# Kernel optimization log

Measured on AMD Instinct MI355X. Metric: run time of the kernel, lower is better.

The kernel has to match this reference:

```python
import jax, jax.numpy as jnp
import numpy as np

D_MODEL = 1024
FEED = 4096
HEADS = 16
EPS = 1e-5


def _ln(x, g, b):
    mu = jnp.mean(x, axis=-1, keepdims=True)
    var = jnp.var(x, axis=-1, keepdims=True)
    return (x - mu) * jax.lax.rsqrt(var + EPS) * g + b


def setup_inputs() -> dict:
    key = jax.random.key(0)
    ks = jax.random.split(key, 8)
    s = 0.02
    return {
        "src": jax.random.normal(ks[0], (8, 512, D_MODEL), jnp.float32),
        "wq": jax.random.normal(ks[1], (D_MODEL, D_MODEL), jnp.float32) * s,
        "bq": jnp.zeros((D_MODEL,), jnp.float32),
        "wk": jax.random.normal(ks[2], (D_MODEL, D_MODEL), jnp.float32) * s,
        "bk": jnp.zeros((D_MODEL,), jnp.float32),
        "wv": jax.random.normal(ks[3], (D_MODEL, D_MODEL), jnp.float32) * s,
        "bv": jnp.zeros((D_MODEL,), jnp.float32),
        "g1": jnp.ones((D_MODEL,), jnp.float32),
        "be1": jnp.zeros((D_MODEL,), jnp.float32),
        "w1": jax.random.normal(ks[4], (D_MODEL, FEED), jnp.float32) * s,
        "b1": jnp.zeros((FEED,), jnp.float32),
        "w2": jax.random.normal(ks[5], (FEED, D_MODEL), jnp.float32) * s,
        "b2": jnp.zeros((D_MODEL,), jnp.float32),
        "g2": jnp.ones((D_MODEL,), jnp.float32),
        "be2": jnp.zeros((D_MODEL,), jnp.float32),
    }


def reference(src, wq, bq, wk, bk, wv, bv, g1, be1, w1, b1, w2, b2, g2, be2):
    bs, seq, d = src.shape
    dk = d // HEADS
    q = src @ wq + bq
    k = src @ wk + bk
    v = src @ wv + bv
    # [B, H, S, dk]
    q = q.reshape(bs, seq, HEADS, dk).transpose(0, 2, 1, 3)
    k = k.reshape(bs, seq, HEADS, dk).transpose(0, 2, 1, 3)
    v = v.reshape(bs, seq, HEADS, dk).transpose(0, 2, 1, 3)
    scores = jnp.einsum('bhqd,bhkd->bhqk', q, k)  # no mask (src_mask unused in original)
    att = jax.nn.softmax(scores / jnp.sqrt(jnp.float32(dk)), axis=-1)
    ctx = jnp.einsum('bhqk,bhkd->bhqd', att, v)
    ctx = ctx.transpose(0, 2, 1, 3).reshape(bs, seq, d)  # concat heads
    x = _ln(ctx + src, g1, be1)
    # FFN (dropout = identity at eval)
    h = jax.nn.relu(x @ w1 + b1)
    y = h @ w2 + b2
    return _ln(y + x, g2, be2)
```

## Files before the change

kernel.cpp:

```cpp
#include <hip/hip_runtime.h>
#include <hip/hip_bf16.h>
#include <stdint.h>

#define DM   1024
#define FF   4096
#define NH   16
#define DK   64
#define SEQ  512
#define NTOK 4096

typedef __attribute__((ext_vector_type(8))) unsigned short ushort8;
typedef __attribute__((ext_vector_type(4))) unsigned short ushort4v;
typedef __attribute__((ext_vector_type(8))) short bf16x8;
typedef __attribute__((ext_vector_type(4))) float f32x4;

__device__ __forceinline__ float bf2f(unsigned short u) {
  union { unsigned int i; float f; } v; v.i = ((unsigned int)u) << 16; return v.f;
}
__device__ __forceinline__ unsigned short f2bf(float f) {
  union { float fl; unsigned int i; } v; v.fl = f;
  v.i += 0x7fffu + ((v.i >> 16) & 1u);
  return (unsigned short)(v.i >> 16);
}

__device__ __forceinline__ void gload16(const unsigned short* g, unsigned short* l) {
  __builtin_amdgcn_global_load_lds(
      (const __attribute__((address_space(1))) unsigned int*)g,
      (__attribute__((address_space(3))) unsigned int*)l, 16, 0, 0);
}

__global__ __launch_bounds__(256)
void prep_kernel(const float* __restrict__ src, unsigned short* __restrict__ srcb,
                 const float* __restrict__ wq, const float* __restrict__ wk,
                 const float* __restrict__ wv, unsigned short* __restrict__ WqkvT,
                 const float* __restrict__ w1, unsigned short* __restrict__ W1T,
                 const float* __restrict__ w2, unsigned short* __restrict__ W2T,
                 const float* __restrict__ bq, const float* __restrict__ bk,
                 const float* __restrict__ bv, float* __restrict__ bqkv) {
  const int z = blockIdx.x;
  const int tid = threadIdx.x;
  if (z < 4096) {
    const long i = ((long)z * 256 + tid) * 4;
    f32x4 v = *(const f32x4*)(src + i);
    ushort4v o;
#pragma unroll
    for (int j = 0; j < 4; j++) o[j] = f2bf(v[j]);
    *(ushort4v*)(srcb + i) = o;
    return;
  }
  if (z >= 15360) {
    const int i = (z - 15360) * 256 + tid;
    if (i < 3072)
      bqkv[i] = (i < 1024) ? bq[i] : ((i < 2048) ? bk[i - 1024] : bv[i - 2048]);
    return;
  }
  const float* in;
  unsigned short* out;
  int ldin, ldout;
  long r0, c0;
  if (z < 7168) {
    const int w = (z - 4096) >> 10;
    const int t = (z - 4096) & 1023;
    in = (w == 0) ? wq : (w == 1) ? wk : wv;
    out = WqkvT + (long)w * 1024 * 1024;
    ldin = 1024; ldout = 1024;
    r0 = (long)(t >> 5) * 32; c0 = (long)(t & 31) * 32;
  } else if (z < 11264) {
    const int t = z - 7168;
    in = w1; out = W1T; ldin = 4096; ldout = 1024;
    r0 = (long)(t >> 7) * 32; c0 = (long)(t & 127) * 32;
  } else {
    const int t = z - 11264;
    in = w2; out = W2T; ldin = 1024; ldout = 4096;
    r0 = (long)(t >> 5) * 32; c0 = (long)(t & 31) * 32;
  }
  __shared__ unsigned short tile[32][33];
  const int tx = tid & 31, ty = tid >> 5;
#pragma unroll
  for (int i = 0; i < 4; i++)
    tile[ty + i * 8][tx] = f2bf(in[(r0 + ty + i * 8) * ldin + c0 + tx]);
  __syncthreads();
#pragma unroll
  for (int i = 0; i < 4; i++)
    out[(c0 + ty + i * 8) * ldout + r0 + tx] = tile[tx][ty + i * 8];
}

template <bool RELU, bool PARTIAL, bool VOUT>
__global__ __launch_bounds__(512, 2)
void gemm256(const unsigned short* __restrict__ A, int lda,
             const unsigned short* __restrict__ B, int ldb,
             const float* __restrict__ bias,
             unsigned short* __restrict__ C,
             unsigned short* __restrict__ P1,
             unsigned short* __restrict__ P2,
             unsigned short* __restrict__ P3,
             int ldc, int nTN) {
  __shared__ unsigned short sm[65536];
  const int tid = threadIdx.x;
  const int lane = tid & 63;
  const int wid = tid >> 6;
  const int wr = wid >> 2, wc = wid & 3;
  const int kgrp = wid >> 2;

  const unsigned int T = gridDim.x;
  const unsigned int q8 = T >> 3;
  const unsigned int x = blockIdx.x;
  const unsigned int swz = (x & 7) * q8 + (x >> 3);
  const long bm = (long)(swz / nTN) * 256;
  const long bn = (long)(swz % nTN) * 256;
  const long kbase = (long)blockIdx.y * 1024;

  f32x4 acc[8][4];
#pragma unroll
  for (int mf = 0; mf < 8; mf++)
#pragma unroll
    for (int nf = 0; nf < 4; nf++) acc[mf][nf] = f32x4{0.f, 0.f, 0.f, 0.f};

  const int strow = tid >> 2;
  const int scol = (((tid & 3) ^ ((tid >> 3) & 3)) << 3);
  const unsigned short* pA = A + (bm + strow) * lda + kbase + scol;
  const unsigned short* pB = B + (bn + strow) * ldb + kbase + scol;
  unsigned short* dA = sm + tid * 8;
  unsigned short* dB = sm + 32768 + tid * 8;

  const int g = lane >> 4;
  int offA[8], offB[4];
#pragma unroll
  for (int mf = 0; mf < 8; mf++) {
    const int rm = wr * 128 + mf * 16 + (lane & 15);
    offA[mf] = rm * 32 + ((g ^ ((rm >> 1) & 3)) << 3);
  }
#pragma unroll
  for (int nf = 0; nf < 4; nf++) {
    const int rb = wc * 64 + nf * 16 + (lane & 15);
    offB[nf] = rb * 32 + ((g ^ ((rb >> 1) & 3)) << 3);
  }

#define GA(kt, ks, rh, bu) gload16(pA + (long)(rh) * 128 * lda + (kt) * 64 + (ks) * 32, \
                                   dA + (bu) * 16384 + (ks) * 8192 + (rh) * 4096)
#define GB(kt, ks, rh, bu) gload16(pB + (long)(rh) * 128 * ldb + (kt) * 64 + (ks) * 32, \
                                   dB + (bu) * 16384 + (ks) * 8192 + (rh) * 4096)
#define MF16(AR, BR, MO)                                                      \
  do {                                                                        \
    __builtin_amdgcn_s_setprio(1);                                            \
    _Pragma("unroll")                                                         \
    for (int mf = 0; mf < 4; mf++)                                            \
      _Pragma("unroll")                                                       \
      for (int nf = 0; nf < 4; nf++)                                          \
        acc[(MO) + mf][nf] = __builtin_amdgcn_mfma_f32_16x16x32_bf16(         \
            AR[mf], BR[nf], acc[(MO) + mf][nf], 0, 0, 0);                     \
    __builtin_amdgcn_s_setprio(0);                                            \
  } while (0)

  GA(0, 0, 0, 0); GA(0, 0, 1, 0); GA(0, 1, 0, 0); GA(0, 1, 1, 0);
  GB(0, 0, 0, 0); GB(0, 0, 1, 0); GB(0, 1, 0, 0); GB(0, 1, 1, 0);

  for (int t = 0; t < 16; ++t) {
    const int c = t & 1, n2 = c ^ 1;
    const int k1 = t + 1;
    const unsigned short* smAc = sm + c * 16384;
    const unsigned short* smBc = sm + 32768 + c * 16384;
    bf16x8 a_[4], bcur[4];
    const int ks0off = kgrp * 8192;
    const int ks1off = (1 - kgrp) * 8192;

    GA(k1, 0, 0, n2); GA(k1, 0, 1, n2);
    asm volatile("s_waitcnt vmcnt(2)\ns_barrier" ::: "memory");
#pragma unroll
    for (int nf = 0; nf < 4; nf++) bcur[nf] = *(const bf16x8*)(smBc + ks0off + offB[nf]);
#pragma unroll
    for (int mf = 0; mf < 4; mf++) a_[mf] = *(const bf16x8*)(smAc + ks0off + offA[mf]);
    MF16(a_, bcur, 0);
    GA(k1, 1, 0, n2); GA(k1, 1, 1, n2);
#pragma unroll
    for (int mf = 0; mf < 4; mf++) a_[mf] = *(const bf16x8*)(smAc + ks0off + offA[4 + mf]);
    asm volatile("s_barrier" ::: "memory");
    MF16(a_, bcur, 4);
    GB(k1, 0, 0, n2); GB(k1, 0, 1, n2);
#pragma unroll
    for (int nf = 0; nf < 4; nf++) bcur[nf] = *(const bf16x8*)(smBc + ks1off + offB[nf]);
#pragma unroll
    for (int mf = 0; mf < 4; mf++) a_[mf] = *(const bf16x8*)(smAc + ks1off + offA[mf]);
    asm volatile("s_barrier" ::: "memory");
    MF16(a_, bcur, 0);
    GB(k1, 1, 0, n2); GB(k1, 1, 1, n2);
#pragma unroll
    for (int mf = 0; mf < 4; mf++) a_[mf] = *(const bf16x8*)(smAc + ks1off + offA[4 + mf]);
    asm volatile("s_waitcnt lgkmcnt(0)\ns_barrier" ::: "memory");
    MF16(a_, bcur, 4);
  }
#undef GA
#undef GB
#undef MF16

  asm volatile("s_waitcnt vmcnt(0)" ::: "memory");

  if (VOUT && bn >= 2048) {
    const int b  = (int)(bm >> 9);
    const int s0 = (int)(bm & 511);
    const int lcol = wc * 64 + (lane & 15);
    const int lrow = wr * 128 + ((lane >> 4) << 2);
#pragma unroll
    for (int nf = 0; nf < 4; nf++) {
      const int gcol = (int)bn + lcol + nf * 16;
      const float bv = bias[gcol];
      const int gc = gcol - 2048;
      const int h = gc >> 6, d = gc & 63;
      unsigned short* vbase = P1 + ((long)(b * 16 + h) * 64 + d) * 512;
#pragma unroll
      for (int mf = 0; mf < 8; mf++) {
        const int s = s0 + lrow + mf * 16;
        ushort4v o;
#pragma unroll
        for (int i = 0; i < 4; i++) o[i] = f2bf(acc[mf][nf][i] + bv);
        *(ushort4v*)(vbase + s) = o;
      }
    }
    return;
  }

  unsigned short* Cw = C;
  if (PARTIAL) {
    const int kc = blockIdx.y;
    Cw = (kc == 0) ? C : (kc == 1) ? P1 : (kc == 2) ? P2 : P3;
  }

  __syncthreads();
  {
    const int lrow = wr * 128 + ((lane >> 4) << 2);
    const int lcol = wc * 64 + (lane & 15);
#pragma unroll
    for (int nf = 0; nf < 4; nf++) {
      const int col = lcol + nf * 16;
      const float bv = PARTIAL ? 0.f : bias[bn + col];
#pragma unroll
      for (int mf = 0; mf < 8; mf++) {
#pragma unroll
        for (int i = 0; i < 4; i++) {
          float v = acc[mf][nf][i] + bv;
          if (RELU) v = fmaxf(v, 0.f);
          sm[(lrow + mf * 16 + i) * 256 + col] = f2bf(v);
        }
      }
    }
  }
  __syncthreads();
  const int srow = tid >> 5;
  const int scol8 = (tid & 31) * 8;
#pragma unroll
  for (int p = 0; p < 16; ++p) {
    const int r = p * 16 + srow;
    ushort8 vrow = *(const ushort8*)(sm + r * 256 + scol8);
    *(ushort8*)(&Cw[(bm + r) * ldc + bn + scol8]) = vrow;
  }
}

__global__ __launch_bounds__(256)
void attn_kernel(const unsigned short* __restrict__ QKV,
                 const unsigned short* __restrict__ Vt,
                 unsigned short* __restrict__ CTX) {
  const int lin = blockIdx.x;
  const int xcd = lin & 7;
  const int slot = lin >> 3;
  const int bh = xcd + 8 * (slot >> 3);
  const int qt = slot & 7;
  const int b = bh >> 4, h = bh & 15;
  const int tid = threadIdx.x;
  const int lane = tid & 63;
  const int wid = tid >> 6;

  __shared__ unsigned short Ks[64][72];
  __shared__ unsigned short Vs[64][72];
  __shared__ unsigned short Ps[4][16][72];

  const int qrow0 = qt * 64 + wid * 16;
  const unsigned short* Qb = QKV + (long)(b * SEQ + qrow0) * 3072 + h * 64;
  bf16x8 aq[2];
#pragma unroll
  for (int ks = 0; ks < 2; ks++)
    aq[ks] = *(const bf16x8*)(Qb + (long)(lane & 15) * 3072 + ks * 32 +
                              (lane >> 4) * 8);

  f32x4 acc_o[4];
#pragma unroll
  for (int n = 0; n < 4; n++) acc_o[n] = f32x4{0.f, 0.f, 0.f, 0.f};
  float rsum[4] = {0.f, 0.f, 0.f, 0.f};

  const int sr = tid >> 3;
  const int sc = (tid & 7) * 8;
  const unsigned short* Kg = QKV + (long)(b * SEQ) * 3072 + 1024 + h * 64 + sc;
  const unsigned short* Vg = Vt + (long)bh * (DK * SEQ) + sc;

  ushort8 kr0 = *(const ushort8*)(Kg + (long)sr * 3072);
  ushort8 kr1 = *(const ushort8*)(Kg + (long)(sr + 32) * 3072);
  ushort8 vr0 = *(const ushort8*)(Vg + (long)sr * SEQ);
  ushort8 vr1 = *(const ushort8*)(Vg + (long)(sr + 32) * SEQ);

#pragma unroll
  for (int c = 0; c < 8; ++c) {
    __syncthreads();
    *(ushort8*)(&Ks[sr][sc]) = kr0;
    *(ushort8*)(&Ks[sr + 32][sc]) = kr1;
    *(ushort8*)(&Vs[sr][sc]) = vr0;
    *(ushort8*)(&Vs[sr + 32][sc]) = vr1;
    if (c < 7) {
      kr0 = *(const ushort8*)(Kg + (long)((c + 1) * 64 + sr) * 3072);
      kr1 = *(const ushort8*)(Kg + (long)((c + 1) * 64 + sr + 32) * 3072);
      vr0 = *(const ushort8*)(Vg + (long)sr * SEQ + (c + 1) * 64);
      vr1 = *(const ushort8*)(Vg + (long)(sr + 32) * SEQ + (c + 1) * 64);
    }
    __syncthreads();

    f32x4 s[4];
#pragma unroll
    for (int n = 0; n < 4; n++) s[n] = f32x4{0.f, 0.f, 0.f, 0.f};
#pragma unroll
    for (int ks = 0; ks < 2; ks++) {
      bf16x8 kf[4];
#pragma unroll
      for (int n = 0; n < 4; n++)
        kf[n] = *(const bf16x8*)(&Ks[n * 16 + (lane & 15)][ks * 32 + (lane >> 4) * 8]);
#pragma unroll
      for (int n = 0; n < 4; n++)
        s[n] = __builtin_amdgcn_mfma_f32_16x16x32_bf16(aq[ks], kf[n], s[n], 0, 0, 0);
    }

#pragma unroll
    for (int n = 0; n < 4; n++) {
#pragma unroll
      for (int i = 0; i < 4; i++) {
        const float p = __expf(s[n][i] * 0.125f);
        rsum[i] += p;
        Ps[wid][(lane >> 4) * 4 + i][n * 16 + (lane & 15)] = f2bf(p);
      }
    }

#pragma unroll
    for (int ks = 0; ks < 2; ks++) {
      bf16x8 pa = *(const bf16x8*)(&Ps[wid][lane & 15][ks * 32 + (lane >> 4) * 8]);
      bf16x8 vf[4];
#pragma unroll
      for (int n = 0; n < 4; n++)
        vf[n] = *(const bf16x8*)(&Vs[n * 16 + (lane & 15)][ks * 32 + (lane >> 4) * 8]);
#pragma unroll
      for (int n = 0; n < 4; n++)
        acc_o[n] = __builtin_amdgcn_mfma_f32_16x16x32_bf16(pa, vf[n], acc_o[n], 0, 0, 0);
    }
  }

#pragma unroll
  for (int i = 0; i < 4; i++) {
#pragma unroll
    for (int off = 1; off < 16; off <<= 1) rsum[i] += __shfl_xor(rsum[i], off, 64);
  }

  const long orow0 = (long)(b * SEQ + qrow0);
#pragma unroll
  for (int i = 0; i < 4; i++) {
    const float inv = 1.f / rsum[i];
    const long r = orow0 + (lane >> 4) * 4 + i;
#pragma unroll
    for (int n = 0; n < 4; n++)
      CTX[r * DM + h * 64 + n * 16 + (lane & 15)] = f2bf(acc_o[n][i] * inv);
  }
}

__global__ __launch_bounds__(256)
void ln1_kernel(const unsigned short* __restrict__ X,
                const unsigned short* __restrict__ R,
                const float* __restrict__ g,
                const float* __restrict__ be,
                unsigned short* __restrict__ Ob) {
  const int t = blockIdx.x;
  const int tid = threadIdx.x;
  const long base = (long)t * DM + tid * 4;
  __shared__ float red[8];

  ushort4v xv = *(const ushort4v*)(X + base);
  ushort4v rv = *(const ushort4v*)(R + base);
  float v[4];
#pragma unroll
  for (int j = 0; j < 4; j++) v[j] = bf2f(xv[j]) + bf2f(rv[j]);
  float s = v[0] + v[1] + v[2] + v[3];
  float q = v[0] * v[0] + v[1] * v[1] + v[2] * v[2] + v[3] * v[3];
#pragma unroll
  for (int off = 1; off < 64; off <<= 1) {
    s += __shfl_xor(s, off, 64);
    q += __shfl_xor(q, off, 64);
  }
  if ((tid & 63) == 0) { red[tid >> 6] = s; red[4 + (tid >> 6)] = q; }
  __syncthreads();
  s = red[0] + red[1] + red[2] + red[3];
  q = red[4] + red[5] + red[6] + red[7];
  const float mu = s * (1.f / DM);
  const float var = q * (1.f / DM) - mu * mu;
  const float rstd = rsqrtf(fmaxf(var, 0.f) + 1e-5f);

  f32x4 gv = *(const f32x4*)(g + tid * 4);
  f32x4 bv = *(const f32x4*)(be + tid * 4);
  ushort4v ob;
#pragma unroll
  for (int j = 0; j < 4; j++)
    ob[j] = f2bf((v[j] - mu) * rstd * gv[j] + bv[j]);
  *(ushort4v*)(Ob + base) = ob;
}

__global__ __launch_bounds__(256)
void ln2_kernel(const unsigned short* __restrict__ P0,
                const unsigned short* __restrict__ P1,
                const unsigned short* __restrict__ P2,
                const unsigned short* __restrict__ P3,
                const float* __restrict__ b2,
                const unsigned short* __restrict__ R,
                const float* __restrict__ g,
                const float* __restrict__ be,
                float* __restrict__ O) {
  const int t = blockIdx.x;
  const int tid = threadIdx.x;
  const long base = (long)t * DM + tid * 4;
  __shared__ float red[8];

  ushort4v p0 = *(const ushort4v*)(P0 + base);
  ushort4v p1 = *(const ushort4v*)(P1 + base);
  ushort4v p2 = *(const ushort4v*)(P2 + base);
  ushort4v p3 = *(const ushort4v*)(P3 + base);
  f32x4 bb = *(const f32x4*)(b2 + tid * 4);
  ushort4v rv = *(const ushort4v*)(R + base);
  float v[4];
#pragma unroll
  for (int j = 0; j < 4; j++)
    v[j] = bf2f(p0[j]) + bf2f(p1[j]) + bf2f(p2[j]) + bf2f(p3[j]) + bb[j] + bf2f(rv[j]);
  float s = v[0] + v[1] + v[2] + v[3];
  float q = v[0] * v[0] + v[1] * v[1] + v[2] * v[2] + v[3] * v[3];
#pragma unroll
  for (int off = 1; off < 64; off <<= 1) {
    s += __shfl_xor(s, off, 64);
    q += __shfl_xor(q, off, 64);
  }
  if ((tid & 63) == 0) { red[tid >> 6] = s; red[4 + (tid >> 6)] = q; }
  __syncthreads();
  s = red[0] + red[1] + red[2] + red[3];
  q = red[4] + red[5] + red[6] + red[7];
  const float mu = s * (1.f / DM);
  const float var = q * (1.f / DM) - mu * mu;
  const float rstd = rsqrtf(fmaxf(var, 0.f) + 1e-5f);

  f32x4 gv = *(const f32x4*)(g + tid * 4);
  f32x4 bv = *(const f32x4*)(be + tid * 4);
  f32x4 of;
#pragma unroll
  for (int j = 0; j < 4; j++) of[j] = (v[j] - mu) * rstd * gv[j] + bv[j];
  *(f32x4*)(O + base) = of;
}

extern "C" void kernel_launch(void* const* d_in, const int* in_sizes, int n_in,
                              void* d_out, int out_size, void* d_ws, size_t ws_size,
                              hipStream_t stream) {
  const float* src = (const float*)d_in[0];
  const float* wq  = (const float*)d_in[1];
  const float* bq  = (const float*)d_in[2];
  const float* wk  = (const float*)d_in[3];
  const float* bk  = (const float*)d_in[4];
  const float* wv  = (const float*)d_in[5];
  const float* bv  = (const float*)d_in[6];
  const float* g1  = (const float*)d_in[7];
  const float* be1 = (const float*)d_in[8];
  const float* w1  = (const float*)d_in[9];
  const float* b1  = (const float*)d_in[10];
  const float* w2  = (const float*)d_in[11];
  const float* b2  = (const float*)d_in[12];
  const float* g2  = (const float*)d_in[13];
  const float* be2 = (const float*)d_in[14];
  float* out = (float*)d_out;

  char* ws = (char*)d_ws;
  const size_t MB = 1024 * 1024;
  unsigned short* srcb  = (unsigned short*)(ws + 0);
  unsigned short* WqkvT = (unsigned short*)(ws + 8 * MB);
  float*          bqkv  = (float*)(ws + 14 * MB);
  unsigned short* W1T   = (unsigned short*)(ws + 15 * MB);
  unsigned short* W2T   = (unsigned short*)(ws + 23 * MB);
  unsigned short* QKV   = (unsigned short*)(ws + 31 * MB);
  unsigned short* Vtb   = (unsigned short*)(ws + 55 * MB);
  unsigned short* CTX   = (unsigned short*)(ws + 63 * MB);
  unsigned short* X1    = (unsigned short*)(ws + 71 * MB);
  unsigned short* Pk3   = (unsigned short*)(ws + 79 * MB);
  unsigned short* Hb    = (unsigned short*)(ws + 31 * MB);
  unsigned short* Pk0   = (unsigned short*)(ws + 0);
  unsigned short* Pk1   = (unsigned short*)(ws + 15 * MB);
  unsigned short* Pk2   = (unsigned short*)(ws + 63 * MB);
  if (ws_size < 87 * MB) return;

  prep_kernel<<<15372, 256, 0, stream>>>(src, srcb, wq, wk, wv, WqkvT,
                                         w1, W1T, w2, W2T, bq, bk, bv, bqkv);

  gemm256<false, false, true><<<dim3(192, 1), 512, 0, stream>>>(
      srcb, 1024, WqkvT, 1024, bqkv, QKV, Vtb, nullptr, nullptr, 3072, 12);
  attn_kernel<<<1024, 256, 0, stream>>>(QKV, Vtb, CTX);
  ln1_kernel<<<NTOK, 256, 0, stream>>>(CTX, srcb, g1, be1, X1);
  gemm256<true, false, false><<<dim3(256, 1), 512, 0, stream>>>(
      X1, 1024, W1T, 1024, b1, Hb, nullptr, nullptr, nullptr, 4096, 16);
  gemm256<false, true, false><<<dim3(64, 4), 512, 0, stream>>>(
      Hb, 4096, W2T, 4096, nullptr, Pk0, Pk1, Pk2, Pk3, 1024, 4);
  ln2_kernel<<<NTOK, 256, 0, stream>>>(Pk0, Pk1, Pk2, Pk3, b2, X1, g2, be2, out);
}
```

Measured before the change: 161.2 us.

## Add dedicated 128x384-tile QKV GEMM kernel to fill all CUs

After: 160.3 us (median of 3 runs). Within noise of the previous version (-0.5%).

```diff
diff --git a/kernel.cpp b/kernel.cpp
--- a/kernel.cpp
+++ b/kernel.cpp
@@ -85,7 +85,7 @@
     out[(c0 + ty + i * 8) * ldout + r0 + tx] = tile[tx][ty + i * 8];
 }
 
-template <bool RELU, bool PARTIAL, bool VOUT>
+template <bool RELU, bool PARTIAL>
 __global__ __launch_bounds__(512, 2)
 void gemm256(const unsigned short* __restrict__ A, int lda,
              const unsigned short* __restrict__ B, int ldb,
@@ -195,30 +195,6 @@
 
   asm volatile("s_waitcnt vmcnt(0)" ::: "memory");
 
-  if (VOUT && bn >= 2048) {
-    const int b  = (int)(bm >> 9);
-    const int s0 = (int)(bm & 511);
-    const int lcol = wc * 64 + (lane & 15);
-    const int lrow = wr * 128 + ((lane >> 4) << 2);
-#pragma unroll
-    for (int nf = 0; nf < 4; nf++) {
-      const int gcol = (int)bn + lcol + nf * 16;
-      const float bv = bias[gcol];
-      const int gc = gcol - 2048;
-      const int h = gc >> 6, d = gc & 63;
-      unsigned short* vbase = P1 + ((long)(b * 16 + h) * 64 + d) * 512;
-#pragma unroll
-      for (int mf = 0; mf < 8; mf++) {
-        const int s = s0 + lrow + mf * 16;
-        ushort4v o;
-#pragma unroll
-        for (int i = 0; i < 4; i++) o[i] = f2bf(acc[mf][nf][i] + bv);
-        *(ushort4v*)(vbase + s) = o;
-      }
-    }
-    return;
-  }
-
   unsigned short* Cw = C;
   if (PARTIAL) {
     const int kc = blockIdx.y;
@@ -252,6 +228,151 @@
     const int r = p * 16 + srow;
     ushort8 vrow = *(const ushort8*)(sm + r * 256 + scol8);
     *(ushort8*)(&Cw[(bm + r) * ldc + bn + scol8]) = vrow;
+  }
+}
+
+__global__ __launch_bounds__(512, 2)
+void gemm_qkv(const unsigned short* __restrict__ A,
+              const unsigned short* __restrict__ B,
+              const float* __restrict__ bias,
+              unsigned short* __restrict__ C,
+              unsigned short* __restrict__ Vt) {
+  __shared__ unsigned short sm[65536];
+  const int tid = threadIdx.x;
+  const int lane = tid & 63;
+  const int wid = tid >> 6;
+
+  const unsigned int x = blockIdx.x;
+  const unsigned int swz = (x & 7) * 32 + (x >> 3);
+  const long bm = (long)(swz >> 3) * 128;
+  const long bn = (long)(swz & 7) * 384;
+
+  f32x4 acc[8][3];
+#pragma unroll
+  for (int mf = 0; mf < 8; mf++)
+#pragma unroll
+    for (int nf = 0; nf < 3; nf++) acc[mf][nf] = f32x4{0.f, 0.f, 0.f, 0.f};
+
+  const int strow = tid >> 2;
+  const int scol = (((tid & 3) ^ ((tid >> 3) & 3)) << 3);
+  const unsigned short* pA = A + (bm + strow) * 1024 + scol;
+  const unsigned short* pB = B + (bn + strow) * 1024 + scol;
+  unsigned short* dA = sm + tid * 8;
+  unsigned short* dB = sm + 16384 + tid * 8;
+
+  const int g = lane >> 4;
+  int offA[8], offB[3];
+#pragma unroll
+  for (int mf = 0; mf < 8; mf++) {
+    const int rm = mf * 16 + (lane & 15);
+    offA[mf] = rm * 32 + ((g ^ ((rm >> 1) & 3)) << 3);
+  }
+#pragma unroll
+  for (int nf = 0; nf < 3; nf++) {
+    const int rb = wid * 48 + nf * 16 + (lane & 15);
+    offB[nf] = rb * 32 + ((g ^ ((rb >> 1) & 3)) << 3);
+  }
+
+#define GAQ(kt, ks, bu) gload16(pA + (kt) * 64 + (ks) * 32,                    \
+                                dA + (bu) * 8192 + (ks) * 4096)
+#define GBQ(kt, ks, rh, bu) gload16(pB + (long)(rh) * 128 * 1024 + (kt) * 64 + (ks) * 32, \
+                                    dB + (bu) * 24576 + (ks) * 12288 + (rh) * 4096)
+#define MFQ(AR, MO)                                                           \
+  do {                                                                        \
+    __builtin_amdgcn_s_setprio(1);                                            \
+    _Pragma("unroll")                                                         \
+    for (int mf = 0; mf < 4; mf++)                                            \
+      _Pragma("unroll")                                                       \
+      for (int nf = 0; nf < 3; nf++)                                          \
+        acc[(MO) + mf][nf] = __builtin_amdgcn_mfma_f32_16x16x32_bf16(         \
+            AR[mf], bcur[nf], acc[(MO) + mf][nf], 0, 0, 0);                   \
+    __builtin_amdgcn_s_setprio(0);                                            \
+  } while (0)
+
+  GAQ(0, 0, 0); GAQ(0, 1, 0);
+  GBQ(0, 0, 0, 0); GBQ(0, 0, 1, 0); GBQ(0, 0, 2, 0);
+  GBQ(0, 1, 0, 0); GBQ(0, 1, 1, 0); GBQ(0, 1, 2, 0);
+
+  for (int t = 0; t < 16; ++t) {
+    const int c = t & 1, n2 = c ^ 1;
+    const int k1 = t + 1;
+    const unsigned short* smA = sm + c * 8192;
+    const unsigned short* smB = sm + 16384 + c * 24576;
+    bf16x8 a_[4], bcur[3];
+
+    GAQ(k1, 0, n2); GAQ(k1, 1, n2);
+    asm volatile("s_waitcnt vmcnt(2)\ns_barrier" ::: "memory");
+#pragma unroll
+    for (int nf = 0; nf < 3; nf++) bcur[nf] = *(const bf16x8*)(smB + offB[nf]);
+#pragma unroll
+    for (int mf = 0; mf < 4; mf++) a_[mf] = *(const bf16x8*)(smA + offA[mf]);
+    MFQ(a_, 0);
+    GBQ(k1, 0, 0, n2); GBQ(k1, 0, 1, n2);
+#pragma unroll
+    for (int mf = 0; mf < 4; mf++) a_[mf] = *(const bf16x8*)(smA + offA[4 + mf]);
+    asm volatile("s_barrier" ::: "memory");
+    MFQ(a_, 4);
+    GBQ(k1, 0, 2, n2); GBQ(k1, 1, 0, n2);
+#pragma unroll
+    for (int nf = 0; nf < 3; nf++) bcur[nf] = *(const bf16x8*)(smB + 12288 + offB[nf]);
+#pragma unroll
+    for (int mf = 0; mf < 4; mf++) a_[mf] = *(const bf16x8*)(smA + 4096 + offA[mf]);
+    asm volatile("s_barrier" ::: "memory");
+    MFQ(a_, 0);
+    GBQ(k1, 1, 1, n2); GBQ(k1, 1, 2, n2);
+#pragma unroll
+    for (int mf = 0; mf < 4; mf++) a_[mf] = *(const bf16x8*)(smA + 4096 + offA[4 + mf]);
+    asm volatile("s_waitcnt lgkmcnt(0)\ns_barrier" ::: "memory");
+    MFQ(a_, 4);
+  }
+#undef GAQ
+#undef GBQ
+#undef MFQ
+
+  asm volatile("s_waitcnt vmcnt(0)" ::: "memory");
+
+  const int bq16 = (int)(bm >> 9) * 16;
+  const int s0 = (int)(bm & 511);
+  const int lrow = (lane >> 4) << 2;
+  const bool anyC = (bn < 2048);
+  if (anyC) __syncthreads();
+
+#pragma unroll
+  for (int nf = 0; nf < 3; nf++) {
+    const int gbase = (int)bn + wid * 48 + nf * 16;
+    const float bv = bias[gbase + (lane & 15)];
+    if (gbase >= 2048) {
+      const int gc = gbase - 2048;
+      const int h = gc >> 6;
+      const int d = (gc & 63) + (lane & 15);
+      unsigned short* vb = Vt + ((long)(bq16 + h) * 64 + d) * 512 + s0 + lrow;
+#pragma unroll
+      for (int mf = 0; mf < 8; mf++) {
+        ushort4v o;
+#pragma unroll
+        for (int i = 0; i < 4; i++) o[i] = f2bf(acc[mf][nf][i] + bv);
+        *(ushort4v*)(vb + mf * 16) = o;
+      }
+    } else {
+      const int lc = wid * 48 + nf * 16 + (lane & 15);
+#pragma unroll
+      for (int mf = 0; mf < 8; mf++) {
+#pragma unroll
+        for (int i = 0; i < 4; i++)
+          sm[(mf * 16 + lrow + i) * 384 + lc] = f2bf(acc[mf][nf][i] + bv);
+      }
+    }
+  }
+
+  if (anyC) {
+    __syncthreads();
+    const int r = tid >> 2;
+    const int nseg = (bn == 1920) ? 4 : 12;
+    for (int p = 0; p < nseg; ++p) {
+      const int seg = p * 4 + (tid & 3);
+      ushort8 v = *(const ushort8*)(sm + r * 384 + seg * 8);
+      *(ushort8*)(&C[(bm + r) * 3072 + bn + seg * 8]) = v;
+    }
   }
 }
 
@@ -494,13 +615,12 @@
   prep_kernel<<<15372, 256, 0, stream>>>(src, srcb, wq, wk, wv, WqkvT,
                                          w1, W1T, w2, W2T, bq, bk, bv, bqkv);
 
-  gemm256<false, false, true><<<dim3(192, 1), 512, 0, stream>>>(
-      srcb, 1024, WqkvT, 1024, bqkv, QKV, Vtb, nullptr, nullptr, 3072, 12);
+  gemm_qkv<<<256, 512, 0, stream>>>(srcb, WqkvT, bqkv, QKV, Vtb);
   attn_kernel<<<1024, 256, 0, stream>>>(QKV, Vtb, CTX);
   ln1_kernel<<<NTOK, 256, 0, stream>>>(CTX, srcb, g1, be1, X1);
-  gemm256<true, false, false><<<dim3(256, 1), 512, 0, stream>>>(
+  gemm256<true, false><<<dim3(256, 1), 512, 0, stream>>>(
       X1, 1024, W1T, 1024, b1, Hb, nullptr, nullptr, nullptr, 4096, 16);
-  gemm256<false, true, false><<<dim3(64, 4), 512, 0, stream>>>(
+  gemm256<false, true><<<dim3(64, 4), 512, 0, stream>>>(
       Hb, 4096, W2T, 4096, nullptr, Pk0, Pk1, Pk2, Pk3, 1024, 4);
   ln2_kernel<<<NTOK, 256, 0, stream>>>(Pk0, Pk1, Pk2, Pk3, b2, X1, g2, be2, out);
 }
```
